# Performance work log

Measured on AMD Instinct MI355X. Metric: run time of the kernel, lower is better.

## Reference

```python
import jax, jax.numpy as jnp
import numpy as np

E = 4          # num_experts
M = 4          # num_modals
C = 512        # in_channels
H1, H2, OUT = 128, 48, 16  # expert hidden/output channels


def setup_inputs() -> dict:
    key = jax.random.key(0)
    ks = jax.random.split(key, 8)
    b, n, t = 16, 4096, 1

    def w(k, shape, fan_in):
        return jax.random.normal(k, shape, jnp.float32) * (1.0 / np.sqrt(fan_in))

    return {
        "x": jax.random.normal(ks[0], (b, C, M, n, t), jnp.float32),
        # stacked expert params: leading axis = expert
        "W1": w(ks[1], (E, H1, C), C),   "b1": jnp.zeros((E, H1), jnp.float32),
        "W2": w(ks[2], (E, H2, H1), H1), "b2": jnp.zeros((E, H2), jnp.float32),
        "W3": w(ks[3], (E, OUT, H2), H2),"b3": jnp.zeros((E, OUT), jnp.float32),
        # gate params
        "Wg1": w(ks[4], (H1, C), C),     "bg1": jnp.zeros((H1,), jnp.float32),
        "Wg2": w(ks[5], (E, H1), H1),    "bg2": jnp.zeros((E,), jnp.float32),
    }


def reference(x, W1, b1, W2, b2, W3, b3, Wg1, bg1, Wg2, bg2):
    b = x.shape[0]
    # gate: AdaptiveAvgPool3d((M,1,1)) == mean over (n,t) since m==M already
    pooled = x.mean(axis=(3, 4))                                   # (b, C, M)
    g = jax.nn.relu(jnp.einsum('oc,bcm->bom', Wg1, pooled) + bg1[None, :, None])
    g = jnp.einsum('oc,bcm->bom', Wg2, g) + bg2[None, :, None]     # (b, E, M)
    # torch: flatten then view(b, num_modals, num_experts) -> row-major reshape
    weights = jax.nn.softmax(g.reshape(b, M, E), axis=2)           # (b, M, E)

    # all experts densely: 1x1x1 convs == channel matmuls, stacked over e
    h = jax.nn.relu(jnp.einsum('eoc,bcmnt->ebomnt', W1, x)
                    + b1[:, None, :, None, None, None])            # (E,b,H1,M,n,t)
    h = jax.nn.relu(jnp.einsum('eoi,ebimnt->ebomnt', W2, h)
                    + b2[:, None, :, None, None, None])            # (E,b,H2,M,n,t)
    h = (jnp.einsum('eoi,ebimnt->ebomnt', W3, h)
         + b3[:, None, :, None, None, None])                       # (E,b,OUT,M,n,t)

    # per-modal weighted combination over experts
    out = jnp.einsum('ebomnt,bme->bomnt', h, weights)              # (b,OUT,M,n,t)
    return out
```

## Files before the change

kernel.cpp:

```cpp
#include <hip/hip_runtime.h>

typedef _Float16 f16;
typedef f16 f16x8 __attribute__((ext_vector_type(8)));
typedef f16 f16x4 __attribute__((ext_vector_type(4)));
typedef f16 f16x2 __attribute__((ext_vector_type(2)));
typedef float f32x4 __attribute__((ext_vector_type(4)));

#define BDIM 16
#define CDIM 512
#define MDIM 4
#define NDIM 4096
#define NB   64
#define NTILES (NDIM/NB)

#define SX(p) ((((p)&7) ^ (((p)>>3)&7)))

__global__ __launch_bounds__(256) void prep_kernel(
    const float* __restrict__ W1, const float* __restrict__ W2, const float* __restrict__ W3,
    f16* __restrict__ W1s, f16* __restrict__ W2s, f16* __restrict__ W3s)
{
  int i = blockIdx.x * 256 + threadIdx.x;
  if (i < 262144) {
    int ki = i & 7; int rest = i >> 3;
    int o = rest & 127; rest >>= 7;
    int kb = rest & 63; int e = rest >> 6;
    W1s[i] = (f16)W1[(e*128 + o)*512 + kb*8 + ki];
  } else if (i < 262144 + 24576) {
    int j = i - 262144;
    int ki = j & 7; int rest = j >> 3;
    int o = rest % 48; rest /= 48;
    int kb = rest & 15; int e = rest >> 4;
    W2s[j] = (f16)W2[(e*48 + o)*128 + kb*8 + ki];
  } else if (i < 262144 + 24576 + 4096) {
    int j = i - 262144 - 24576;
    int ki = j & 7; int rest = j >> 3;
    int o = rest & 15; rest >>= 4;
    int kb = rest & 7; int e = rest >> 3;
    int k = kb*8 + ki;
    W3s[j] = (k < 48) ? (f16)W3[(e*16 + o)*48 + k] : (f16)0.f;
  }
}

__global__ __launch_bounds__(256) void pool_kernel(const float* __restrict__ x,
                                                   float* __restrict__ pooled)
{
  __shared__ float red[4];
  const int tid = threadIdx.x;
  const float* row = x + (size_t)blockIdx.x * NDIM;
  float s = 0.f;
  #pragma unroll
  for (int it = 0; it < 4; ++it) {
    float4 v = *(const float4*)(row + it*1024 + tid*4);
    s += v.x + v.y + v.z + v.w;
  }
  #pragma unroll
  for (int off = 32; off; off >>= 1) s += __shfl_down(s, off);
  if ((tid & 63) == 0) red[tid >> 6] = s;
  __syncthreads();
  if (tid == 0) pooled[blockIdx.x] = (red[0]+red[1]+red[2]+red[3]) * (1.0f/4096.0f);
}

__global__ __launch_bounds__(256) void gate_kernel(
    const float* __restrict__ pooled, const float* __restrict__ Wg1,
    const float* __restrict__ bg1, const float* __restrict__ Wg2,
    const float* __restrict__ bg2, float* __restrict__ wgt)
{
  __shared__ float pl[512*4];
  __shared__ float g1[128*4];
  __shared__ float g2[16];
  const int b = blockIdx.x, tid = threadIdx.x;
  for (int i = tid; i < 2048; i += 256) pl[i] = pooled[b*2048 + i];
  __syncthreads();
  #pragma unroll
  for (int u = 0; u < 2; ++u) {
    int idx = u*256 + tid;
    int o = idx >> 2, mm = idx & 3;
    float acc = bg1[o];
    for (int c = 0; c < 512; ++c) acc += Wg1[o*512 + c] * pl[c*4 + mm];
    g1[o*4 + mm] = fmaxf(acc, 0.f);
  }
  __syncthreads();
  if (tid < 16) {
    int e = tid >> 2, mm = tid & 3;
    float acc = bg2[e];
    for (int o = 0; o < 128; ++o) acc += Wg2[e*128 + o] * g1[o*4 + mm];
    g2[e*4 + mm] = acc;
  }
  __syncthreads();
  if (tid < 4) {
    int mrow = tid;
    float v0 = g2[mrow*4+0], v1 = g2[mrow*4+1], v2 = g2[mrow*4+2], v3 = g2[mrow*4+3];
    float mx = fmaxf(fmaxf(v0,v1), fmaxf(v2,v3));
    float e0 = expf(v0-mx), e1 = expf(v1-mx), e2 = expf(v2-mx), e3 = expf(v3-mx);
    float inv = 1.0f / (e0+e1+e2+e3);
    wgt[b*16 + mrow*4 + 0] = e0*inv;
    wgt[b*16 + mrow*4 + 1] = e1*inv;
    wgt[b*16 + mrow*4 + 2] = e2*inv;
    wgt[b*16 + mrow*4 + 3] = e3*inv;
  }
}

__global__ __launch_bounds__(512, 4) void moe_kernel(
    const float* __restrict__ x,
    const f16* __restrict__ W1s, const f16* __restrict__ W2s, const f16* __restrict__ W3s,
    const float* __restrict__ b1, const float* __restrict__ b2, const float* __restrict__ b3,
    const float* __restrict__ wgt, float* __restrict__ out)
{
  __shared__ __align__(16) char smem[40960];
  char* Xs0 = smem;
  char* Xs1 = smem + 8192;
  char* H1t = smem + 16384;
  char* H2t = smem + 32768;

  const int tid  = threadIdx.x;
  const int bid  = blockIdx.x;
  const int tile = bid & 63;
  const int m    = (bid >> 6) & 3;
  const int b    = bid >> 8;

  ((uint4*)H2t)[tid] = make_uint4(0u,0u,0u,0u);

  const int wave = tid >> 6, lane = tid & 63;
  const int g = lane >> 4, r = lane & 15;
  const int o0 = wave * 16;

  const int cp = tid >> 4;
  const int q  = tid & 15;
  const float* xb = x + ((size_t)(b*2048 + m)) * 4096 + (size_t)tile*64
                      + (size_t)(2*cp)*16384 + q*4;

  {
    f32x4 v0 = *(const f32x4*)xb;
    f32x4 v1 = *(const f32x4*)(xb + 16384);
    #pragma unroll
    for (int i = 0; i < 4; ++i) {
      int p = q*4 + i;
      f16x2 hv; hv[0] = (f16)v0[i]; hv[1] = (f16)v1[i];
      *(f16x2*)(Xs0 + p*128 + ((4*cp) ^ (SX(p)<<4))) = hv;
    }
  }

  f32x4 acc[4][4];
  #pragma unroll
  for (int e = 0; e < 4; ++e)
    #pragma unroll
    for (int pt = 0; pt < 4; ++pt) acc[e][pt] = (f32x4){0.f,0.f,0.f,0.f};

  for (int ck = 0; ck < 8; ++ck) {
    __syncthreads();
    f32x4 nv0, nv1;
    if (ck < 7) {
      const float* src = xb + (size_t)(ck+1)*64*16384;
      nv0 = *(const f32x4*)src;
      nv1 = *(const f32x4*)(src + 16384);
    }
    const char* Xb = (ck & 1) ? Xs1 : Xs0;
    #pragma unroll
    for (int ks = 0; ks < 2; ++ks) {
      const int kbl = ks*4 + g;
      const int kbg = ck*8 + kbl;
      f16x8 bf[4];
      #pragma unroll
      for (int pt = 0; pt < 4; ++pt) {
        int p = pt*16 + r;
        bf[pt] = *(const f16x8*)(Xb + p*128 + ((kbl*16) ^ (SX(p)<<4)));
      }
      #pragma unroll
      for (int e = 0; e < 4; ++e) {
        f16x8 a = *(const f16x8*)(W1s + ((size_t)((e*64 + kbg)*128) + o0 + r)*8);
        #pragma unroll
        for (int pt = 0; pt < 4; ++pt)
          acc[e][pt] = __builtin_amdgcn_mfma_f32_16x16x32_f16(a, bf[pt], acc[e][pt], 0, 0, 0);
      }
    }
    if (ck < 7) {
      char* dst = (ck & 1) ? Xs0 : Xs1;
      #pragma unroll
      for (int i = 0; i < 4; ++i) {
        int p = q*4 + i;
        f16x2 hv; hv[0] = (f16)nv0[i]; hv[1] = (f16)nv1[i];
        *(f16x2*)(dst + p*128 + ((4*cp) ^ (SX(p)<<4))) = hv;
      }
    }
  }

  f32x4 outacc = {0.f, 0.f, 0.f, 0.f};
  for (int e = 0; e < 4; ++e) {
    {
      const f32x4 bias = *(const f32x4*)(b1 + e*128 + o0 + g*4);
      const int ob = (o0 + g*4) * 2;
      #pragma unroll
      for (int pt = 0; pt < 4; ++pt) {
        int p = pt*16 + r;
        f16x4 h;
        #pragma unroll
        for (int j = 0; j < 4; ++j) h[j] = (f16)fmaxf(acc[e][pt][j] + bias[j], 0.f);
        *(f16x4*)(H1t + p*256 + (ob ^ (SX(p)<<4))) = h;
      }
    }
    __syncthreads();

    #pragma unroll
    for (int s = 0; s < 2; ++s) {
      int f = wave + s*8;
      if (f < 12) {
        int ot = f >> 2, pt = f & 3;
        int p = pt*16 + r;
        f32x4 acc2 = {0.f,0.f,0.f,0.f};
        #pragma unroll
        for (int ks = 0; ks < 4; ++ks) {
          int kb = ks*4 + g;
          f16x8 a  = *(const f16x8*)(W2s + (size_t)((e*16 + kb)*48 + ot*16 + r)*8);
          f16x8 bf = *(const f16x8*)(H1t + p*256 + ((kb*16) ^ (SX(p)<<4)));
          acc2 = __builtin_amdgcn_mfma_f32_16x16x32_f16(a, bf, acc2, 0, 0, 0);
        }
        const f32x4 bias = *(const f32x4*)(b2 + e*48 + ot*16 + g*4);
        const int ob = (ot*16 + g*4) * 2;
        f16x4 h;
        #pragma unroll
        for (int j = 0; j < 4; ++j) h[j] = (f16)fmaxf(acc2[j] + bias[j], 0.f);
        *(f16x4*)(H2t + p*128 + (ob ^ (SX(p)<<4))) = h;
      }
    }
    __syncthreads();

    if (wave < 4) {
      const int pt = wave;
      int p = pt*16 + r;
      f32x4 acc3 = {0.f,0.f,0.f,0.f};
      #pragma unroll
      for (int ks = 0; ks < 2; ++ks) {
        int kb = ks*4 + g;
        f16x8 a  = *(const f16x8*)(W3s + (size_t)((e*8 + kb)*16 + r)*8);
        f16x8 bf = *(const f16x8*)(H2t + p*128 + ((kb*16) ^ (SX(p)<<4)));
        acc3 = __builtin_amdgcn_mfma_f32_16x16x32_f16(a, bf, acc3, 0, 0, 0);
      }
      const float w_e = wgt[(b*4 + m)*4 + e];
      const f32x4 bias = *(const f32x4*)(b3 + e*16 + g*4);
      #pragma unroll
      for (int j = 0; j < 4; ++j) outacc[j] += w_e * (acc3[j] + bias[j]);
    }
  }

  if (wave < 4) {
    const int pt = wave;
    #pragma unroll
    for (int reg = 0; reg < 4; ++reg) {
      int o = g*4 + reg;
      out[(((size_t)b*16 + o)*4 + m)*4096 + (size_t)tile*64 + pt*16 + r] = outacc[reg];
    }
  }
}

extern "C" void kernel_launch(void* const* d_in, const int* in_sizes, int n_in,
                              void* d_out, int out_size, void* d_ws, size_t ws_size,
                              hipStream_t stream) {
  const float* x   = (const float*)d_in[0];
  const float* W1  = (const float*)d_in[1];
  const float* b1  = (const float*)d_in[2];
  const float* W2  = (const float*)d_in[3];
  const float* b2  = (const float*)d_in[4];
  const float* W3  = (const float*)d_in[5];
  const float* b3  = (const float*)d_in[6];
  const float* Wg1 = (const float*)d_in[7];
  const float* bg1 = (const float*)d_in[8];
  const float* Wg2 = (const float*)d_in[9];
  const float* bg2 = (const float*)d_in[10];
  float* out = (float*)d_out;

  char* ws = (char*)d_ws;
  float* pooled = (float*)ws;
  float* wgt    = (float*)(ws + 131072);
  f16* W1s = (f16*)(ws + 132096);
  f16* W2s = (f16*)(ws + 132096 + 524288);
  f16* W3s = (f16*)(ws + 132096 + 524288 + 49152);

  prep_kernel<<<(262144 + 24576 + 4096 + 255)/256, 256, 0, stream>>>(W1, W2, W3, W1s, W2s, W3s);
  pool_kernel<<<BDIM*CDIM*MDIM, 256, 0, stream>>>(x, pooled);
  gate_kernel<<<BDIM, 256, 0, stream>>>(pooled, Wg1, bg1, Wg2, bg2, wgt);
  moe_kernel<<<BDIM*MDIM*NTILES, 512, 0, stream>>>(x, W1s, W2s, W3s, b1, b2, b3, wgt, out);
}
```

Baseline: 412.1 us.

## Fuse pooling into MoE kernel and defer gating to a combine pass

```diff
diff --git a/kernel.cpp b/kernel.cpp
--- a/kernel.cpp
+++ b/kernel.cpp
@@ -12,6 +12,7 @@
 #define NDIM 4096
 #define NB   64
 #define NTILES (NDIM/NB)
+#define NBMT  (BDIM*MDIM*NTILES)
 
 #define SX(p) ((((p)&7) ^ (((p)>>3)&7)))
 
@@ -41,70 +42,11 @@
   }
 }
 
-__global__ __launch_bounds__(256) void pool_kernel(const float* __restrict__ x,
-                                                   float* __restrict__ pooled)
-{
-  __shared__ float red[4];
-  const int tid = threadIdx.x;
-  const float* row = x + (size_t)blockIdx.x * NDIM;
-  float s = 0.f;
-  #pragma unroll
-  for (int it = 0; it < 4; ++it) {
-    float4 v = *(const float4*)(row + it*1024 + tid*4);
-    s += v.x + v.y + v.z + v.w;
-  }
-  #pragma unroll
-  for (int off = 32; off; off >>= 1) s += __shfl_down(s, off);
-  if ((tid & 63) == 0) red[tid >> 6] = s;
-  __syncthreads();
-  if (tid == 0) pooled[blockIdx.x] = (red[0]+red[1]+red[2]+red[3]) * (1.0f/4096.0f);
-}
-
-__global__ __launch_bounds__(256) void gate_kernel(
-    const float* __restrict__ pooled, const float* __restrict__ Wg1,
-    const float* __restrict__ bg1, const float* __restrict__ Wg2,
-    const float* __restrict__ bg2, float* __restrict__ wgt)
-{
-  __shared__ float pl[512*4];
-  __shared__ float g1[128*4];
-  __shared__ float g2[16];
-  const int b = blockIdx.x, tid = threadIdx.x;
-  for (int i = tid; i < 2048; i += 256) pl[i] = pooled[b*2048 + i];
-  __syncthreads();
-  #pragma unroll
-  for (int u = 0; u < 2; ++u) {
-    int idx = u*256 + tid;
-    int o = idx >> 2, mm = idx & 3;
-    float acc = bg1[o];
-    for (int c = 0; c < 512; ++c) acc += Wg1[o*512 + c] * pl[c*4 + mm];
-    g1[o*4 + mm] = fmaxf(acc, 0.f);
-  }
-  __syncthreads();
-  if (tid < 16) {
-    int e = tid >> 2, mm = tid & 3;
-    float acc = bg2[e];
-    for (int o = 0; o < 128; ++o) acc += Wg2[e*128 + o] * g1[o*4 + mm];
-    g2[e*4 + mm] = acc;
-  }
-  __syncthreads();
-  if (tid < 4) {
-    int mrow = tid;
-    float v0 = g2[mrow*4+0], v1 = g2[mrow*4+1], v2 = g2[mrow*4+2], v3 = g2[mrow*4+3];
-    float mx = fmaxf(fmaxf(v0,v1), fmaxf(v2,v3));
-    float e0 = expf(v0-mx), e1 = expf(v1-mx), e2 = expf(v2-mx), e3 = expf(v3-mx);
-    float inv = 1.0f / (e0+e1+e2+e3);
-    wgt[b*16 + mrow*4 + 0] = e0*inv;
-    wgt[b*16 + mrow*4 + 1] = e1*inv;
-    wgt[b*16 + mrow*4 + 2] = e2*inv;
-    wgt[b*16 + mrow*4 + 3] = e3*inv;
-  }
-}
-
-__global__ __launch_bounds__(512, 4) void moe_kernel(
+__global__ __launch_bounds__(512, 2) void moe_kernel(
     const float* __restrict__ x,
     const f16* __restrict__ W1s, const f16* __restrict__ W2s, const f16* __restrict__ W3s,
     const float* __restrict__ b1, const float* __restrict__ b2, const float* __restrict__ b3,
-    const float* __restrict__ wgt, float* __restrict__ out)
+    float* __restrict__ partial, f16* __restrict__ h3)
 {
   __shared__ __align__(16) char smem[40960];
   char* Xs0 = smem;
@@ -128,6 +70,7 @@
   const int q  = tid & 15;
   const float* xb = x + ((size_t)(b*2048 + m)) * 4096 + (size_t)tile*64
                       + (size_t)(2*cp)*16384 + q*4;
+  float* prow = partial + (size_t)bid*512 + 2*cp;
 
   {
     f32x4 v0 = *(const f32x4*)xb;
@@ -138,6 +81,14 @@
       f16x2 hv; hv[0] = (f16)v0[i]; hv[1] = (f16)v1[i];
       *(f16x2*)(Xs0 + p*128 + ((4*cp) ^ (SX(p)<<4))) = hv;
     }
+    float s0 = v0[0]+v0[1]+v0[2]+v0[3];
+    float s1 = v1[0]+v1[1]+v1[2]+v1[3];
+    #pragma unroll
+    for (int off = 8; off; off >>= 1) {
+      s0 += __shfl_down(s0, off, 16);
+      s1 += __shfl_down(s1, off, 16);
+    }
+    if (q == 0) { float2 sv = {s0, s1}; *(float2*)prow = sv; }
   }
 
   f32x4 acc[4][4];
@@ -181,10 +132,18 @@
         f16x2 hv; hv[0] = (f16)nv0[i]; hv[1] = (f16)nv1[i];
         *(f16x2*)(dst + p*128 + ((4*cp) ^ (SX(p)<<4))) = hv;
       }
-    }
-  }
-
-  f32x4 outacc = {0.f, 0.f, 0.f, 0.f};
+      float s0 = nv0[0]+nv0[1]+nv0[2]+nv0[3];
+      float s1 = nv1[0]+nv1[1]+nv1[2]+nv1[3];
+      #pragma unroll
+      for (int off = 8; off; off >>= 1) {
+        s0 += __shfl_down(s0, off, 16);
+        s1 += __shfl_down(s1, off, 16);
+      }
+      if (q == 0) { float2 sv = {s0, s1}; *(float2*)(prow + (ck+1)*64) = sv; }
+    }
+  }
+
+  #pragma unroll
   for (int e = 0; e < 4; ++e) {
     {
       const f32x4 bias = *(const f32x4*)(b1 + e*128 + o0 + g*4);
@@ -235,21 +194,87 @@
         f16x8 bf = *(const f16x8*)(H2t + p*128 + ((kb*16) ^ (SX(p)<<4)));
         acc3 = __builtin_amdgcn_mfma_f32_16x16x32_f16(a, bf, acc3, 0, 0, 0);
       }
-      const float w_e = wgt[(b*4 + m)*4 + e];
       const f32x4 bias = *(const f32x4*)(b3 + e*16 + g*4);
       #pragma unroll
-      for (int j = 0; j < 4; ++j) outacc[j] += w_e * (acc3[j] + bias[j]);
-    }
-  }
-
-  if (wave < 4) {
-    const int pt = wave;
-    #pragma unroll
-    for (int reg = 0; reg < 4; ++reg) {
-      int o = g*4 + reg;
-      out[(((size_t)b*16 + o)*4 + m)*4096 + (size_t)tile*64 + pt*16 + r] = outacc[reg];
-    }
-  }
+      for (int j = 0; j < 4; ++j) {
+        int o = g*4 + j;
+        h3[(((size_t)(e*NBMT + bid))*16 + o)*64 + pt*16 + r] = (f16)(acc3[j] + bias[j]);
+      }
+    }
+  }
+}
+
+__global__ __launch_bounds__(256) void gate_kernel(
+    const float* __restrict__ partial, const float* __restrict__ Wg1,
+    const float* __restrict__ bg1, const float* __restrict__ Wg2,
+    const float* __restrict__ bg2, float* __restrict__ wgt)
+{
+  __shared__ float pl[512*4];
+  __shared__ float g1[128*4];
+  __shared__ float g2[16];
+  const int b = blockIdx.x, tid = threadIdx.x;
+
+  const int c0 = tid * 2;
+  #pragma unroll
+  for (int mm = 0; mm < 4; ++mm) {
+    const float* base = partial + ((size_t)((b*4 + mm)*64))*512 + c0;
+    float a0 = 0.f, a1 = 0.f;
+    for (int tl = 0; tl < 64; ++tl) {
+      float2 v = *(const float2*)(base + tl*512);
+      a0 += v.x; a1 += v.y;
+    }
+    pl[(c0+0)*4 + mm] = a0 * (1.0f/4096.0f);
+    pl[(c0+1)*4 + mm] = a1 * (1.0f/4096.0f);
+  }
+  __syncthreads();
+
+  #pragma unroll
+  for (int u = 0; u < 2; ++u) {
+    int idx = u*256 + tid;
+    int o = idx >> 2, mm = idx & 3;
+    float acc = bg1[o];
+    for (int c = 0; c < 512; ++c) acc += Wg1[o*512 + c] * pl[c*4 + mm];
+    g1[o*4 + mm] = fmaxf(acc, 0.f);
+  }
+  __syncthreads();
+  if (tid < 16) {
+    int e = tid >> 2, mm = tid & 3;
+    float acc = bg2[e];
+    for (int o = 0; o < 128; ++o) acc += Wg2[e*128 + o] * g1[o*4 + mm];
+    g2[e*4 + mm] = acc;
+  }
+  __syncthreads();
+  if (tid < 4) {
+    int mrow = tid;
+    float v0 = g2[mrow*4+0], v1 = g2[mrow*4+1], v2 = g2[mrow*4+2], v3 = g2[mrow*4+3];
+    float mx = fmaxf(fmaxf(v0,v1), fmaxf(v2,v3));
+    float e0 = expf(v0-mx), e1 = expf(v1-mx), e2 = expf(v2-mx), e3 = expf(v3-mx);
+    float inv = 1.0f / (e0+e1+e2+e3);
+    wgt[b*16 + mrow*4 + 0] = e0*inv;
+    wgt[b*16 + mrow*4 + 1] = e1*inv;
+    wgt[b*16 + mrow*4 + 2] = e2*inv;
+    wgt[b*16 + mrow*4 + 3] = e3*inv;
+  }
+}
+
+__global__ __launch_bounds__(256) void combine_kernel(
+    const f16* __restrict__ h3, const float* __restrict__ wgt,
+    float* __restrict__ out)
+{
+  const int bmt = blockIdx.x;
+  const int tile = bmt & 63, m = (bmt >> 6) & 3, b = bmt >> 8;
+  const int t = threadIdx.x;
+  const int o = t >> 4, pq = t & 15;
+
+  const f32x4 w = *(const f32x4*)(wgt + (b*4 + m)*4);
+  f32x4 s = {0.f, 0.f, 0.f, 0.f};
+  #pragma unroll
+  for (int e = 0; e < 4; ++e) {
+    f16x4 h = *(const f16x4*)(h3 + (((size_t)(e*NBMT + bmt))*16 + o)*64 + pq*4);
+    #pragma unroll
+    for (int j = 0; j < 4; ++j) s[j] += w[e] * (float)h[j];
+  }
+  *(f32x4*)(out + (((size_t)b*16 + o)*4 + m)*4096 + tile*64 + pq*4) = s;
 }
 
 extern "C" void kernel_launch(void* const* d_in, const int* in_sizes, int n_in,
@@ -269,14 +294,15 @@
   float* out = (float*)d_out;
 
   char* ws = (char*)d_ws;
-  float* pooled = (float*)ws;
-  float* wgt    = (float*)(ws + 131072);
-  f16* W1s = (f16*)(ws + 132096);
-  f16* W2s = (f16*)(ws + 132096 + 524288);
-  f16* W3s = (f16*)(ws + 132096 + 524288 + 49152);
+  float* wgt    = (float*)ws;
+  f16* W1s      = (f16*)(ws + 4096);
+  f16* W2s      = (f16*)(ws + 4096 + 524288);
+  f16* W3s      = (f16*)(ws + 4096 + 524288 + 49152);
+  float* partial= (float*)(ws + (1u<<20));
+  f16* h3       = (f16*)(ws + (16u<<20));
 
   prep_kernel<<<(262144 + 24576 + 4096 + 255)/256, 256, 0, stream>>>(W1, W2, W3, W1s, W2s, W3s);
-  pool_kernel<<<BDIM*CDIM*MDIM, 256, 0, stream>>>(x, pooled);
-  gate_kernel<<<BDIM, 256, 0, stream>>>(pooled, Wg1, bg1, Wg2, bg2, wgt);
-  moe_kernel<<<BDIM*MDIM*NTILES, 512, 0, stream>>>(x, W1s, W2s, W3s, b1, b2, b3, wgt, out);
-}
+  moe_kernel<<<NBMT, 512, 0, stream>>>(x, W1s, W2s, W3s, b1, b2, b3, partial, h3);
+  gate_kernel<<<BDIM, 256, 0, stream>>>(partial, Wg1, bg1, Wg2, bg2, wgt);
+  combine_kernel<<<NBMT, 256, 0, stream>>>(h3, wgt, out);
+}
```

New measurement: 625.3 us. +51.8%, slower.
